# Performance work log

Hardware: AMD Instinct MI355X
Metric: run time of the kernel (lower is better)

The kernel has to match this reference:

```python
import jax, jax.numpy as jnp
import numpy as np
import math

H = 8          # num_heads
DV = 1024      # dim_V
LN_EPS = 1e-5


def _layernorm(x, g, b):
    mu = jnp.mean(x, axis=-1, keepdims=True)
    var = jnp.mean(jnp.square(x - mu), axis=-1, keepdims=True)
    return (x - mu) * jax.lax.rsqrt(var + LN_EPS) * g + b


def setup_inputs() -> dict:
    key = jax.random.key(0)
    ks = jax.random.split(key, 12)
    B, NQ, NK, DQ, DK = 4, 2048, 2048, 1024, 1024
    s = 0.02
    return {
        "Q": jax.random.normal(ks[0], (B, NQ, DQ), jnp.float32),
        "K": jax.random.normal(ks[1], (B, NK, DK), jnp.float32),
        "Wq": jax.random.normal(ks[2], (DV, DQ), jnp.float32) * s,
        "bq": jnp.zeros((DV,), jnp.float32),
        "Wk": jax.random.normal(ks[3], (DV, DK), jnp.float32) * s,
        "bk": jnp.zeros((DV,), jnp.float32),
        "Wv": jax.random.normal(ks[4], (DV, DK), jnp.float32) * s,
        "bv": jnp.zeros((DV,), jnp.float32),
        "Wo": jax.random.normal(ks[5], (DV, DV), jnp.float32) * s,
        "bo": jnp.zeros((DV,), jnp.float32),
        "g0": jnp.ones((DV,), jnp.float32),
        "b0": jnp.zeros((DV,), jnp.float32),
        "g1": jnp.ones((DV,), jnp.float32),
        "b1": jnp.zeros((DV,), jnp.float32),
    }


def reference(Q, K, Wq, bq, Wk, bk, Wv, bv, Wo, bo, g0, b0, g1, b1):
    B, NQ, _ = Q.shape
    NK = K.shape[1]
    d = DV // H  # per-head dim
    # projections
    q = (Q @ Wq.T + bq).reshape(B, NQ, H, d)
    k = (K @ Wk.T + bk).reshape(B, NK, H, d)
    v = (K @ Wv.T + bv).reshape(B, NK, H, d)
    # attention per head (split along feature dim == head split in torch code)
    logits = jnp.einsum('bqhd,bkhd->bhqk', q, k) / math.sqrt(d)
    A = jax.nn.softmax(logits, axis=-1)
    o = q + jnp.einsum('bhqk,bkhd->bqhd', A, v)  # residual with projected Q
    O = o.reshape(B, NQ, DV)
    O = _layernorm(O, g0, b0)
    O = O + jax.nn.relu(O @ Wo.T + bo)
    O = _layernorm(O, g1, b1)
    return O
```

## Files before the change

### kernel.cpp

```cpp
#include <hip/hip_runtime.h>
#include <hip/hip_bf16.h>

typedef __bf16 bf16_t;
typedef __bf16 bf16x8 __attribute__((ext_vector_type(8)));
typedef __bf16 bf16x4 __attribute__((ext_vector_type(4)));
typedef float f32x4 __attribute__((ext_vector_type(4)));

#define B_DIM 4
#define NQ 2048
#define NK 2048
#define DMODEL 1024
#define NH 8
#define DHEAD 128

#define AS1 __attribute__((address_space(1)))
#define AS3 __attribute__((address_space(3)))

__device__ __forceinline__ void gl_lds16(const void* g, void* l) {
    __builtin_amdgcn_global_load_lds((const AS1 void*)g, (AS3 void*)l, 16, 0, 0);
}

struct CvtArgs {
    const float* s[6];
    bf16_t* d[6];
    int n[6];
};

__global__ __launch_bounds__(256) void cvt_k(CvtArgs a) {
    const int p = blockIdx.y;
    const float* s = a.s[p];
    bf16_t* d = a.d[p];
    const int n = a.n[p];
    const int stride = gridDim.x * 256 * 8;
    for (int i = (blockIdx.x * 256 + threadIdx.x) * 8; i < n; i += stride) {
        float4 x0 = *(const float4*)(s + i);
        float4 x1 = *(const float4*)(s + i + 4);
        bf16x8 o = {(bf16_t)x0.x, (bf16_t)x0.y, (bf16_t)x0.z, (bf16_t)x0.w,
                    (bf16_t)x1.x, (bf16_t)x1.y, (bf16_t)x1.z, (bf16_t)x1.w};
        *(bf16x8*)(d + i) = o;
    }
}

__global__ __launch_bounds__(256) void proj_k(
    const bf16_t* Qc, const bf16_t* Kc,
    const bf16_t* Wqc, const bf16_t* Wkc, const bf16_t* Wvc,
    const float* bq, const float* bk, const float* bv,
    bf16_t* qbb, bf16_t* kbb, bf16_t* vT)
{
    const int K = DMODEL, N = DMODEL;
    const int z = blockIdx.z;
    const bf16_t* A  = (z == 0) ? Qc : Kc;
    const bf16_t* Bw = (z == 0) ? Wqc : (z == 1) ? Wkc : Wvc;
    const float* bias = (z == 0) ? bq : (z == 1) ? bk : bv;
    bf16_t* Cb = (z == 0) ? qbb : (z == 1) ? kbb : vT;

    const int tid  = threadIdx.x;
    const int lane = tid & 63;
    const int wv   = tid >> 6;
    const int l16  = lane & 15;
    const int quad = (lane >> 4) & 3;
    const int kc4  = lane >> 4;
    const int wr   = wv >> 1, wc = wv & 1;
    const int rowBase = blockIdx.y * 128;
    const int colBase = blockIdx.x * 128;

    __shared__ bf16_t sA[4096];
    __shared__ bf16_t sB[4096];

    const bf16_t* gA = A + (size_t)(rowBase + wv * 32 + l16) * K + kc4 * 8;
    const bf16_t* gB = Bw + (size_t)(colBase + wv * 32 + l16) * K + kc4 * 8;
    bf16_t* lA0 = &sA[(wv * 2) * 512];
    bf16_t* lA1 = &sA[(wv * 2 + 1) * 512];
    bf16_t* lB0 = &sB[(wv * 2) * 512];
    bf16_t* lB1 = &sB[(wv * 2 + 1) * 512];

    const f32x4 fz = {0.f, 0.f, 0.f, 0.f};
    f32x4 acc[4][4];
#pragma unroll
    for (int i = 0; i < 4; i++)
#pragma unroll
        for (int j = 0; j < 4; j++) acc[i][j] = fz;

    for (int k0 = 0; k0 < K; k0 += 32) {
        gl_lds16(gA, lA0);
        gl_lds16(gA + (size_t)16 * K, lA1);
        gl_lds16(gB, lB0);
        gl_lds16(gB + (size_t)16 * K, lB1);
        gA += 32; gB += 32;
        __syncthreads();

        bf16x8 aF[4], bF[4];
#pragma unroll
        for (int mi = 0; mi < 4; mi++)
            aF[mi] = *(const bf16x8*)(&sA[(wr * 4 + mi) * 512 + (quad * 16 + l16) * 8]);
#pragma unroll
        for (int ni = 0; ni < 4; ni++)
            bF[ni] = *(const bf16x8*)(&sB[(wc * 4 + ni) * 512 + (quad * 16 + l16) * 8]);
#pragma unroll
        for (int mi = 0; mi < 4; mi++)
#pragma unroll
            for (int ni = 0; ni < 4; ni++)
                acc[mi][ni] = __builtin_amdgcn_mfma_f32_16x16x32_bf16(
                    aF[mi], bF[ni], acc[mi][ni], 0, 0, 0);
        __syncthreads();
    }

#pragma unroll
    for (int mi = 0; mi < 4; mi++) {
#pragma unroll
        for (int ni = 0; ni < 4; ni++) {
            int row0 = rowBase + wr * 64 + mi * 16 + quad * 4;
            int col  = colBase + wc * 64 + ni * 16 + l16;
            float bvv = bias[col];
            if (z != 2) {
#pragma unroll
                for (int r = 0; r < 4; r++)
                    Cb[(size_t)(row0 + r) * N + col] = (bf16_t)(acc[mi][ni][r] + bvv);
            } else {
                int b  = row0 >> 11;
                int n0 = row0 & 2047;
                int hh = col >> 7;
                int dd = col & 127;
                bf16x4 p = {(bf16_t)(acc[mi][ni][0] + bvv), (bf16_t)(acc[mi][ni][1] + bvv),
                            (bf16_t)(acc[mi][ni][2] + bvv), (bf16_t)(acc[mi][ni][3] + bvv)};
                *(bf16x4*)(Cb + (size_t)((b * NH + hh) * DHEAD + dd) * NK + n0) = p;
            }
        }
    }
}

__global__ __launch_bounds__(256) void gemm_wo(
    const bf16_t* __restrict__ A, const bf16_t* __restrict__ Bw,
    const float* __restrict__ bias, const float* resid, float* Cf, int M, int N, int K)
{
    const int tid  = threadIdx.x;
    const int lane = tid & 63;
    const int wv   = tid >> 6;
    const int l16  = lane & 15;
    const int quad = (lane >> 4) & 3;
    const int kc4  = lane >> 4;
    const int wr   = wv >> 1, wc = wv & 1;
    const int rowBase = blockIdx.y * 128;
    const int colBase = blockIdx.x * 128;

    __shared__ bf16_t sA[4096];
    __shared__ bf16_t sB[4096];

    const bf16_t* gA = A + (size_t)(rowBase + wv * 32 + l16) * K + kc4 * 8;
    const bf16_t* gB = Bw + (size_t)(colBase + wv * 32 + l16) * K + kc4 * 8;
    bf16_t* lA0 = &sA[(wv * 2) * 512];
    bf16_t* lA1 = &sA[(wv * 2 + 1) * 512];
    bf16_t* lB0 = &sB[(wv * 2) * 512];
    bf16_t* lB1 = &sB[(wv * 2 + 1) * 512];

    const f32x4 fz = {0.f, 0.f, 0.f, 0.f};
    f32x4 acc[4][4];
#pragma unroll
    for (int i = 0; i < 4; i++)
#pragma unroll
        for (int j = 0; j < 4; j++) acc[i][j] = fz;

    for (int k0 = 0; k0 < K; k0 += 32) {
        gl_lds16(gA, lA0);
        gl_lds16(gA + (size_t)16 * K, lA1);
        gl_lds16(gB, lB0);
        gl_lds16(gB + (size_t)16 * K, lB1);
        gA += 32; gB += 32;
        __syncthreads();

        bf16x8 aF[4], bF[4];
#pragma unroll
        for (int mi = 0; mi < 4; mi++)
            aF[mi] = *(const bf16x8*)(&sA[(wr * 4 + mi) * 512 + (quad * 16 + l16) * 8]);
#pragma unroll
        for (int ni = 0; ni < 4; ni++)
            bF[ni] = *(const bf16x8*)(&sB[(wc * 4 + ni) * 512 + (quad * 16 + l16) * 8]);
#pragma unroll
        for (int mi = 0; mi < 4; mi++)
#pragma unroll
            for (int ni = 0; ni < 4; ni++)
                acc[mi][ni] = __builtin_amdgcn_mfma_f32_16x16x32_bf16(
                    aF[mi], bF[ni], acc[mi][ni], 0, 0, 0);
        __syncthreads();
    }

#pragma unroll
    for (int mi = 0; mi < 4; mi++) {
#pragma unroll
        for (int ni = 0; ni < 4; ni++) {
            int row0 = rowBase + wr * 64 + mi * 16 + quad * 4;
            int col  = colBase + wc * 64 + ni * 16 + l16;
            float bvv = bias[col];
#pragma unroll
            for (int r = 0; r < 4; r++) {
                float v = acc[mi][ni][r] + bvv;
                v = v > 0.f ? v : 0.f;
                Cf[(size_t)(row0 + r) * N + col] =
                    resid[(size_t)(row0 + r) * N + col] + v;
            }
        }
    }
}

__global__ __launch_bounds__(128, 2) void attn_k(
    const bf16_t* __restrict__ qb, const bf16_t* __restrict__ kb,
    const bf16_t* __restrict__ vT, float* __restrict__ O)
{
    const int tid  = threadIdx.x;
    const int lane = tid & 63;
    const int wv   = tid >> 6;
    const int l16  = lane & 15;
    const int quad = (lane >> 4) & 3;
    const int bh   = blockIdx.x;
    const int b    = bh >> 3;
    const int h    = bh & 7;
    const int qt   = blockIdx.y * 64;
    const int qrow0 = b * NQ + qt + wv * 32;

    __shared__ bf16_t sK[8192];
    __shared__ bf16_t sV[8192];

    bf16x8 qF[2][4];
#pragma unroll
    for (int qq = 0; qq < 2; qq++)
#pragma unroll
        for (int c = 0; c < 4; c++)
            qF[qq][c] = *(const bf16x8*)(qb + (size_t)(qrow0 + qq * 16 + l16) * DMODEL +
                                         h * DHEAD + c * 32 + quad * 8);

    const f32x4 fz = {0.f, 0.f, 0.f, 0.f};
    f32x4 accO[8][2];
#pragma unroll
    for (int db = 0; db < 8; db++)
#pragma unroll
        for (int qq = 0; qq < 2; qq++) accO[db][qq] = fz;
    float mq[2] = {-3e38f, -3e38f};
    float lq[2] = {0.f, 0.f};
    const float SC2 = 0.08838834764831845f * 1.44269504089f;

    const bf16_t* gKb = kb + ((size_t)b * NK + l16) * DMODEL + h * DHEAD + quad * 8;
    const bf16_t* gVb = vT + ((size_t)bh * DHEAD + l16) * NK + quad * 8;
    const int qa   = (quad & 1) * 2;
    const int srcA = l16 + 16 * qa;
    const int srcB = srcA + 16;
    const bool hi  = (quad >> 1) != 0;

    for (int kt = 0; kt < NK; kt += 64) {
#pragma unroll
        for (int kb2 = 0; kb2 < 2; kb2++) {
            const int kbi = wv * 2 + kb2;
#pragma unroll
            for (int c = 0; c < 4; c++)
                gl_lds16(gKb + (size_t)(kt + kbi * 16) * DMODEL + c * 32,
                         &sK[(kbi * 4 + c) * 512]);
        }
#pragma unroll
        for (int db2 = 0; db2 < 4; db2++) {
            const int dbi = wv * 4 + db2;
#pragma unroll
            for (int kc = 0; kc < 2; kc++)
                gl_lds16(gVb + (size_t)(dbi * 16) * NK + kt + kc * 32,
                         &sV[(dbi * 2 + kc) * 512]);
        }
        __syncthreads();

        f32x4 S[4][2];
#pragma unroll
        for (int kb4 = 0; kb4 < 4; kb4++) {
            S[kb4][0] = fz; S[kb4][1] = fz;
#pragma unroll
            for (int c = 0; c < 4; c++) {
                bf16x8 kF = *(const bf16x8*)(&sK[(kb4 * 4 + c) * 512 + lane * 8]);
                S[kb4][0] = __builtin_amdgcn_mfma_f32_16x16x32_bf16(kF, qF[0][c], S[kb4][0], 0, 0, 0);
                S[kb4][1] = __builtin_amdgcn_mfma_f32_16x16x32_bf16(kF, qF[1][c], S[kb4][1], 0, 0, 0);
            }
        }

        float alph[2];
#pragma unroll
        for (int qq = 0; qq < 2; qq++) {
            float mx = fmaxf(fmaxf(fmaxf(S[0][qq][0], S[0][qq][1]), fmaxf(S[0][qq][2], S[0][qq][3])),
                       fmaxf(fmaxf(S[1][qq][0], S[1][qq][1]), fmaxf(S[1][qq][2], S[1][qq][3])));
            mx = fmaxf(mx, fmaxf(fmaxf(fmaxf(S[2][qq][0], S[2][qq][1]), fmaxf(S[2][qq][2], S[2][qq][3])),
                           fmaxf(fmaxf(S[3][qq][0], S[3][qq][1]), fmaxf(S[3][qq][2], S[3][qq][3]))));
            mx = fmaxf(mx, __shfl_xor(mx, 16));
            mx = fmaxf(mx, __shfl_xor(mx, 32));
            float mn = fmaxf(mq[qq], mx);
            float al = exp2f((mq[qq] - mn) * SC2);
            mq[qq] = mn;
            float mc = mn * SC2;
            float sum = 0.f;
#pragma unroll
            for (int kb4 = 0; kb4 < 4; kb4++)
#pragma unroll
                for (int r = 0; r < 4; r++) {
                    float p = exp2f(fmaf(S[kb4][qq][r], SC2, -mc));
                    S[kb4][qq][r] = p;
                    sum += p;
                }
            lq[qq] = lq[qq] * al + sum;
            alph[qq] = al;
        }
#pragma unroll
        for (int db = 0; db < 8; db++)
#pragma unroll
            for (int qq = 0; qq < 2; qq++)
#pragma unroll
                for (int r = 0; r < 4; r++) accO[db][qq][r] *= alph[qq];

        uint2 pk[4][2];
#pragma unroll
        for (int kb4 = 0; kb4 < 4; kb4++)
#pragma unroll
            for (int qq = 0; qq < 2; qq++) {
                bf16x4 t = {(bf16_t)S[kb4][qq][0], (bf16_t)S[kb4][qq][1],
                            (bf16_t)S[kb4][qq][2], (bf16_t)S[kb4][qq][3]};
                pk[kb4][qq] = __builtin_bit_cast(uint2, t);
            }
        bf16x8 pF[2][2];
#pragma unroll
        for (int kc = 0; kc < 2; kc++)
#pragma unroll
            for (int qq = 0; qq < 2; qq++) {
                unsigned a0 = (unsigned)__shfl((int)pk[2 * kc][qq].x, srcA);
                unsigned b0 = (unsigned)__shfl((int)pk[2 * kc + 1][qq].x, srcA);
                unsigned a1 = (unsigned)__shfl((int)pk[2 * kc][qq].y, srcA);
                unsigned b1 = (unsigned)__shfl((int)pk[2 * kc + 1][qq].y, srcA);
                unsigned a2 = (unsigned)__shfl((int)pk[2 * kc][qq].x, srcB);
                unsigned b2 = (unsigned)__shfl((int)pk[2 * kc + 1][qq].x, srcB);
                unsigned a3 = (unsigned)__shfl((int)pk[2 * kc][qq].y, srcB);
                unsigned b3 = (unsigned)__shfl((int)pk[2 * kc + 1][qq].y, srcB);
                uint4 w = {hi ? b0 : a0, hi ? b1 : a1, hi ? b2 : a2, hi ? b3 : a3};
                pF[kc][qq] = __builtin_bit_cast(bf16x8, w);
            }

#pragma unroll
        for (int kc = 0; kc < 2; kc++)
#pragma unroll
            for (int db = 0; db < 8; db++) {
                bf16x8 vF = *(const bf16x8*)(&sV[(db * 2 + kc) * 512 + lane * 8]);
                accO[db][0] = __builtin_amdgcn_mfma_f32_16x16x32_bf16(vF, pF[kc][0], accO[db][0], 0, 0, 0);
                accO[db][1] = __builtin_amdgcn_mfma_f32_16x16x32_bf16(vF, pF[kc][1], accO[db][1], 0, 0, 0);
            }
        __syncthreads();
    }

    float inv[2];
#pragma unroll
    for (int qq = 0; qq < 2; qq++) {
        float s = lq[qq];
        s += __shfl_xor(s, 16);
        s += __shfl_xor(s, 32);
        inv[qq] = 1.0f / s;
    }

#pragma unroll
    for (int qq = 0; qq < 2; qq++) {
        const int grow = qrow0 + qq * 16 + l16;
#pragma unroll
        for (int db = 0; db < 8; db++) {
            const int gcol = h * DHEAD + db * 16 + quad * 4;
            bf16x4 qr = *(const bf16x4*)(qb + (size_t)grow * DMODEL + gcol);
            f32x4 o;
#pragma unroll
            for (int r = 0; r < 4; r++)
                o[r] = accO[db][qq][r] * inv[qq] + (float)qr[r];
            *(f32x4*)(O + (size_t)grow * DMODEL + gcol) = o;
        }
    }
}

__global__ __launch_bounds__(256) void ln_k(
    const float* __restrict__ X, const float* __restrict__ g,
    const float* __restrict__ bta, float* __restrict__ Yf, bf16_t* Yb)
{
    const int row = blockIdx.x;
    const int t = threadIdx.x;
    float4 x = *(const float4*)(X + (size_t)row * DMODEL + t * 4);
    float s  = x.x + x.y + x.z + x.w;
    float sq = x.x * x.x + x.y * x.y + x.z * x.z + x.w * x.w;
#pragma unroll
    for (int o = 1; o < 64; o <<= 1) {
        s  += __shfl_xor(s, o);
        sq += __shfl_xor(sq, o);
    }
    __shared__ float ls[8];
    int w = t >> 6, ln = t & 63;
    if (ln == 0) { ls[w] = s; ls[4 + w] = sq; }
    __syncthreads();
    s  = ls[0] + ls[1] + ls[2] + ls[3];
    sq = ls[4] + ls[5] + ls[6] + ls[7];
    float mu  = s * (1.f / DMODEL);
    float var = sq * (1.f / DMODEL) - mu * mu;
    float rs  = rsqrtf(var + 1e-5f);
    float4 gv = *(const float4*)(g + t * 4);
    float4 bv = *(const float4*)(bta + t * 4);
    float4 y;
    y.x = (x.x - mu) * rs * gv.x + bv.x;
    y.y = (x.y - mu) * rs * gv.y + bv.y;
    y.z = (x.z - mu) * rs * gv.z + bv.z;
    y.w = (x.w - mu) * rs * gv.w + bv.w;
    *(float4*)(Yf + (size_t)row * DMODEL + t * 4) = y;
    if (Yb) {
        bf16x4 yb = {(bf16_t)y.x, (bf16_t)y.y, (bf16_t)y.z, (bf16_t)y.w};
        *(bf16x4*)(Yb + (size_t)row * DMODEL + t * 4) = yb;
    }
}

extern "C" void kernel_launch(void* const* d_in, const int* in_sizes, int n_in,
                              void* d_out, int out_size, void* d_ws, size_t ws_size,
                              hipStream_t stream)
{
    const float* Q  = (const float*)d_in[0];
    const float* Kx = (const float*)d_in[1];
    const float* Wq = (const float*)d_in[2];
    const float* bq = (const float*)d_in[3];
    const float* Wk = (const float*)d_in[4];
    const float* bk = (const float*)d_in[5];
    const float* Wv = (const float*)d_in[6];
    const float* bv = (const float*)d_in[7];
    const float* Wo = (const float*)d_in[8];
    const float* bo = (const float*)d_in[9];
    const float* g0 = (const float*)d_in[10];
    const float* b0 = (const float*)d_in[11];
    const float* g1 = (const float*)d_in[12];
    const float* b1 = (const float*)d_in[13];
    float* out = (float*)d_out;

    char* ws = (char*)d_ws;
    bf16_t* Qc  = (bf16_t*)(ws);
    bf16_t* Kc  = (bf16_t*)(ws + 16777216);
    bf16_t* Wqc = (bf16_t*)(ws + 33554432);
    bf16_t* Wkc = (bf16_t*)(ws + 35651584);
    bf16_t* Wvc = (bf16_t*)(ws + 37748736);
    bf16_t* Woc = (bf16_t*)(ws + 39845888);
    bf16_t* qbb = (bf16_t*)(ws + 41943040);
    bf16_t* kbb = (bf16_t*)(ws + 58720256);
    bf16_t* vT  = (bf16_t*)(ws + 75497472);
    float*  Obuf = (float*)(ws + 92274688);
    float*  Lf  = (float*)(ws);
    bf16_t* Lb  = kbb;

    CvtArgs ca;
    ca.s[0] = Q;  ca.d[0] = Qc;  ca.n[0] = B_DIM * NQ * DMODEL;
    ca.s[1] = Kx; ca.d[1] = Kc;  ca.n[1] = B_DIM * NK * DMODEL;
    ca.s[2] = Wq; ca.d[2] = Wqc; ca.n[2] = DMODEL * DMODEL;
    ca.s[3] = Wk; ca.d[3] = Wkc; ca.n[3] = DMODEL * DMODEL;
    ca.s[4] = Wv; ca.d[4] = Wvc; ca.n[4] = DMODEL * DMODEL;
    ca.s[5] = Wo; ca.d[5] = Woc; ca.n[5] = DMODEL * DMODEL;
    cvt_k<<<dim3(512, 6), 256, 0, stream>>>(ca);

    const int M = B_DIM * NQ;

    proj_k<<<dim3(DMODEL / 128, M / 128, 3), 256, 0, stream>>>(
        Qc, Kc, Wqc, Wkc, Wvc, bq, bk, bv, qbb, kbb, vT);

    attn_k<<<dim3(B_DIM * NH, NQ / 64), 128, 0, stream>>>(qbb, kbb, vT, Obuf);

    ln_k<<<dim3(M), 256, 0, stream>>>(Obuf, g0, b0, Lf, Lb);

    gemm_wo<<<dim3(DMODEL / 128, M / 128), 256, 0, stream>>>(
        Lb, Woc, bo, Lf, Lf, M, DMODEL, DMODEL);

    ln_k<<<dim3(M), 256, 0, stream>>>(Lf, g1, b1, out, nullptr);
}
```

Baseline: 460.8 us.

## Double-buffer B/K tiles in LDS and load A/V operands directly from global

The GEMM kernels are merged into a templated core. Only the weight tile is staged through LDS, now double-buffered with the next tile's async load issued before the current compute, and A fragments are read straight from global into registers. The attention kernel likewise double-buffers K tiles in LDS and loads V fragments directly from global, cutting one barrier per iteration. The aim is to overlap memory latency with MFMA work and halve synchronization, at the cost of uncoalesced global register loads and more register pressure.

Result: slower. 564.1 us (+22.4%).

```diff
diff --git a/kernel.cpp b/kernel.cpp
--- a/kernel.cpp
+++ b/kernel.cpp
@@ -41,19 +41,12 @@
     }
 }
 
-__global__ __launch_bounds__(256) void proj_k(
-    const bf16_t* Qc, const bf16_t* Kc,
-    const bf16_t* Wqc, const bf16_t* Wkc, const bf16_t* Wvc,
-    const float* bq, const float* bk, const float* bv,
-    bf16_t* qbb, bf16_t* kbb, bf16_t* vT)
-{
-    const int K = DMODEL, N = DMODEL;
-    const int z = blockIdx.z;
-    const bf16_t* A  = (z == 0) ? Qc : Kc;
-    const bf16_t* Bw = (z == 0) ? Wqc : (z == 1) ? Wkc : Wvc;
-    const float* bias = (z == 0) ? bq : (z == 1) ? bk : bv;
-    bf16_t* Cb = (z == 0) ? qbb : (z == 1) ? kbb : vT;
-
+template <int MODE>
+__device__ __forceinline__ void gemm_core(
+    const bf16_t* A, const bf16_t* Bw, const float* bias, const float* resid,
+    bf16_t* Cb, float* Cf, int N, int rowBase, int colBase, bf16_t (*sB)[4096])
+{
+    const int K = DMODEL;
     const int tid  = threadIdx.x;
     const int lane = tid & 63;
     const int wv   = tid >> 6;
@@ -61,18 +54,9 @@
     const int quad = (lane >> 4) & 3;
     const int kc4  = lane >> 4;
     const int wr   = wv >> 1, wc = wv & 1;
-    const int rowBase = blockIdx.y * 128;
-    const int colBase = blockIdx.x * 128;
-
-    __shared__ bf16_t sA[4096];
-    __shared__ bf16_t sB[4096];
-
-    const bf16_t* gA = A + (size_t)(rowBase + wv * 32 + l16) * K + kc4 * 8;
+
     const bf16_t* gB = Bw + (size_t)(colBase + wv * 32 + l16) * K + kc4 * 8;
-    bf16_t* lA0 = &sA[(wv * 2) * 512];
-    bf16_t* lA1 = &sA[(wv * 2 + 1) * 512];
-    bf16_t* lB0 = &sB[(wv * 2) * 512];
-    bf16_t* lB1 = &sB[(wv * 2 + 1) * 512];
+    const bf16_t* gA = A + (size_t)(rowBase + wr * 64 + l16) * K + quad * 8;
 
     const f32x4 fz = {0.f, 0.f, 0.f, 0.f};
     f32x4 acc[4][4];
@@ -81,28 +65,32 @@
 #pragma unroll
         for (int j = 0; j < 4; j++) acc[i][j] = fz;
 
-    for (int k0 = 0; k0 < K; k0 += 32) {
-        gl_lds16(gA, lA0);
-        gl_lds16(gA + (size_t)16 * K, lA1);
-        gl_lds16(gB, lB0);
-        gl_lds16(gB + (size_t)16 * K, lB1);
-        gA += 32; gB += 32;
+    gl_lds16(gB,                  &sB[0][(wv * 2) * 512]);
+    gl_lds16(gB + (size_t)16 * K, &sB[0][(wv * 2 + 1) * 512]);
+    gB += 32;
+
+    for (int t = 0; t < 32; t++) {
         __syncthreads();
-
-        bf16x8 aF[4], bF[4];
+        const int cur = t & 1;
+        bf16x8 aF[4];
 #pragma unroll
         for (int mi = 0; mi < 4; mi++)
-            aF[mi] = *(const bf16x8*)(&sA[(wr * 4 + mi) * 512 + (quad * 16 + l16) * 8]);
+            aF[mi] = *(const bf16x8*)(gA + (size_t)mi * 16 * K + t * 32);
+        if (t + 1 < 32) {
+            gl_lds16(gB,                  &sB[cur ^ 1][(wv * 2) * 512]);
+            gl_lds16(gB + (size_t)16 * K, &sB[cur ^ 1][(wv * 2 + 1) * 512]);
+            gB += 32;
+        }
+        bf16x8 bF[4];
 #pragma unroll
         for (int ni = 0; ni < 4; ni++)
-            bF[ni] = *(const bf16x8*)(&sB[(wc * 4 + ni) * 512 + (quad * 16 + l16) * 8]);
+            bF[ni] = *(const bf16x8*)(&sB[cur][(wc * 4 + ni) * 512 + (quad * 16 + l16) * 8]);
 #pragma unroll
         for (int mi = 0; mi < 4; mi++)
 #pragma unroll
             for (int ni = 0; ni < 4; ni++)
                 acc[mi][ni] = __builtin_amdgcn_mfma_f32_16x16x32_bf16(
                     aF[mi], bF[ni], acc[mi][ni], 0, 0, 0);
-        __syncthreads();
     }
 
 #pragma unroll
@@ -112,10 +100,18 @@
             int row0 = rowBase + wr * 64 + mi * 16 + quad * 4;
             int col  = colBase + wc * 64 + ni * 16 + l16;
             float bvv = bias[col];
-            if (z != 2) {
+            if (MODE == 0) {
 #pragma unroll
                 for (int r = 0; r < 4; r++)
                     Cb[(size_t)(row0 + r) * N + col] = (bf16_t)(acc[mi][ni][r] + bvv);
+            } else if (MODE == 1) {
+#pragma unroll
+                for (int r = 0; r < 4; r++) {
+                    float v = acc[mi][ni][r] + bvv;
+                    v = v > 0.f ? v : 0.f;
+                    Cf[(size_t)(row0 + r) * N + col] =
+                        resid[(size_t)(row0 + r) * N + col] + v;
+                }
             } else {
                 int b  = row0 >> 11;
                 int n0 = row0 & 2047;
@@ -129,77 +125,31 @@
     }
 }
 
+__global__ __launch_bounds__(256) void proj_k(
+    const bf16_t* Qc, const bf16_t* Kc,
+    const bf16_t* Wqc, const bf16_t* Wkc, const bf16_t* Wvc,
+    const float* bq, const float* bk, const float* bv,
+    bf16_t* qbb, bf16_t* kbb, bf16_t* vT)
+{
+    __shared__ bf16_t sB[2][4096];
+    const int z = blockIdx.z;
+    const int rowBase = blockIdx.y * 128;
+    const int colBase = blockIdx.x * 128;
+    if (z == 0)
+        gemm_core<0>(Qc, Wqc, bq, nullptr, qbb, nullptr, DMODEL, rowBase, colBase, sB);
+    else if (z == 1)
+        gemm_core<0>(Kc, Wkc, bk, nullptr, kbb, nullptr, DMODEL, rowBase, colBase, sB);
+    else
+        gemm_core<2>(Kc, Wvc, bv, nullptr, vT, nullptr, DMODEL, rowBase, colBase, sB);
+}
+
 __global__ __launch_bounds__(256) void gemm_wo(
     const bf16_t* __restrict__ A, const bf16_t* __restrict__ Bw,
-    const float* __restrict__ bias, const float* resid, float* Cf, int M, int N, int K)
-{
-    const int tid  = threadIdx.x;
-    const int lane = tid & 63;
-    const int wv   = tid >> 6;
-    const int l16  = lane & 15;
-    const int quad = (lane >> 4) & 3;
-    const int kc4  = lane >> 4;
-    const int wr   = wv >> 1, wc = wv & 1;
-    const int rowBase = blockIdx.y * 128;
-    const int colBase = blockIdx.x * 128;
-
-    __shared__ bf16_t sA[4096];
-    __shared__ bf16_t sB[4096];
-
-    const bf16_t* gA = A + (size_t)(rowBase + wv * 32 + l16) * K + kc4 * 8;
-    const bf16_t* gB = Bw + (size_t)(colBase + wv * 32 + l16) * K + kc4 * 8;
-    bf16_t* lA0 = &sA[(wv * 2) * 512];
-    bf16_t* lA1 = &sA[(wv * 2 + 1) * 512];
-    bf16_t* lB0 = &sB[(wv * 2) * 512];
-    bf16_t* lB1 = &sB[(wv * 2 + 1) * 512];
-
-    const f32x4 fz = {0.f, 0.f, 0.f, 0.f};
-    f32x4 acc[4][4];
-#pragma unroll
-    for (int i = 0; i < 4; i++)
-#pragma unroll
-        for (int j = 0; j < 4; j++) acc[i][j] = fz;
-
-    for (int k0 = 0; k0 < K; k0 += 32) {
-        gl_lds16(gA, lA0);
-        gl_lds16(gA + (size_t)16 * K, lA1);
-        gl_lds16(gB, lB0);
-        gl_lds16(gB + (size_t)16 * K, lB1);
-        gA += 32; gB += 32;
-        __syncthreads();
-
-        bf16x8 aF[4], bF[4];
-#pragma unroll
-        for (int mi = 0; mi < 4; mi++)
-            aF[mi] = *(const bf16x8*)(&sA[(wr * 4 + mi) * 512 + (quad * 16 + l16) * 8]);
-#pragma unroll
-        for (int ni = 0; ni < 4; ni++)
-            bF[ni] = *(const bf16x8*)(&sB[(wc * 4 + ni) * 512 + (quad * 16 + l16) * 8]);
-#pragma unroll
-        for (int mi = 0; mi < 4; mi++)
-#pragma unroll
-            for (int ni = 0; ni < 4; ni++)
-                acc[mi][ni] = __builtin_amdgcn_mfma_f32_16x16x32_bf16(
-                    aF[mi], bF[ni], acc[mi][ni], 0, 0, 0);
-        __syncthreads();
-    }
-
-#pragma unroll
-    for (int mi = 0; mi < 4; mi++) {
-#pragma unroll
-        for (int ni = 0; ni < 4; ni++) {
-            int row0 = rowBase + wr * 64 + mi * 16 + quad * 4;
-            int col  = colBase + wc * 64 + ni * 16 + l16;
-            float bvv = bias[col];
-#pragma unroll
-            for (int r = 0; r < 4; r++) {
-                float v = acc[mi][ni][r] + bvv;
-                v = v > 0.f ? v : 0.f;
-                Cf[(size_t)(row0 + r) * N + col] =
-                    resid[(size_t)(row0 + r) * N + col] + v;
-            }
-        }
-    }
+    const float* __restrict__ bias, const float* resid, float* Cf)
+{
+    __shared__ bf16_t sB[2][4096];
+    gemm_core<1>(A, Bw, bias, resid, nullptr, Cf, DMODEL,
+                 blockIdx.y * 128, blockIdx.x * 128, sB);
 }
 
 __global__ __launch_bounds__(128, 2) void attn_k(
@@ -217,8 +167,7 @@
     const int qt   = blockIdx.y * 64;
     const int qrow0 = b * NQ + qt + wv * 32;
 
-    __shared__ bf16_t sK[8192];
-    __shared__ bf16_t sV[8192];
+    __shared__ bf16_t sK[2][8192];
 
     bf16x8 qF[2][4];
 #pragma unroll
@@ -245,24 +194,37 @@
     const int srcB = srcA + 16;
     const bool hi  = (quad >> 1) != 0;
 
-    for (int kt = 0; kt < NK; kt += 64) {
-#pragma unroll
-        for (int kb2 = 0; kb2 < 2; kb2++) {
-            const int kbi = wv * 2 + kb2;
-#pragma unroll
-            for (int c = 0; c < 4; c++)
-                gl_lds16(gKb + (size_t)(kt + kbi * 16) * DMODEL + c * 32,
-                         &sK[(kbi * 4 + c) * 512]);
-        }
-#pragma unroll
-        for (int db2 = 0; db2 < 4; db2++) {
-            const int dbi = wv * 4 + db2;
+#pragma unroll
+    for (int kb2 = 0; kb2 < 2; kb2++) {
+        const int kbi = wv * 2 + kb2;
+#pragma unroll
+        for (int c = 0; c < 4; c++)
+            gl_lds16(gKb + (size_t)(kbi * 16) * DMODEL + c * 32, &sK[0][(kbi * 4 + c) * 512]);
+    }
+
+    for (int it = 0; it < NK / 64; it++) {
+        __syncthreads();
+        const int cur = it & 1;
+        const int kt = it * 64;
+
+        bf16x8 vF[8][2];
+#pragma unroll
+        for (int db = 0; db < 8; db++)
 #pragma unroll
             for (int kc = 0; kc < 2; kc++)
-                gl_lds16(gVb + (size_t)(dbi * 16) * NK + kt + kc * 32,
-                         &sV[(dbi * 2 + kc) * 512]);
-        }
-        __syncthreads();
+                vF[db][kc] = *(const bf16x8*)(gVb + (size_t)(db * 16) * NK + kt + kc * 32);
+
+        if (it + 1 < NK / 64) {
+            const size_t ko = (size_t)(kt + 64);
+#pragma unroll
+            for (int kb2 = 0; kb2 < 2; kb2++) {
+                const int kbi = wv * 2 + kb2;
+#pragma unroll
+                for (int c = 0; c < 4; c++)
+                    gl_lds16(gKb + (ko + kbi * 16) * DMODEL + c * 32,
+                             &sK[cur ^ 1][(kbi * 4 + c) * 512]);
+            }
+        }
 
         f32x4 S[4][2];
 #pragma unroll
@@ -270,7 +232,7 @@
             S[kb4][0] = fz; S[kb4][1] = fz;
 #pragma unroll
             for (int c = 0; c < 4; c++) {
-                bf16x8 kF = *(const bf16x8*)(&sK[(kb4 * 4 + c) * 512 + lane * 8]);
+                bf16x8 kF = *(const bf16x8*)(&sK[cur][(kb4 * 4 + c) * 512 + lane * 8]);
                 S[kb4][0] = __builtin_amdgcn_mfma_f32_16x16x32_bf16(kF, qF[0][c], S[kb4][0], 0, 0, 0);
                 S[kb4][1] = __builtin_amdgcn_mfma_f32_16x16x32_bf16(kF, qF[1][c], S[kb4][1], 0, 0, 0);
             }
@@ -338,11 +300,9 @@
         for (int kc = 0; kc < 2; kc++)
 #pragma unroll
             for (int db = 0; db < 8; db++) {
-                bf16x8 vF = *(const bf16x8*)(&sV[(db * 2 + kc) * 512 + lane * 8]);
-                accO[db][0] = __builtin_amdgcn_mfma_f32_16x16x32_bf16(vF, pF[kc][0], accO[db][0], 0, 0, 0);
-                accO[db][1] = __builtin_amdgcn_mfma_f32_16x16x32_bf16(vF, pF[kc][1], accO[db][1], 0, 0, 0);
-            }
-        __syncthreads();
+                accO[db][0] = __builtin_amdgcn_mfma_f32_16x16x32_bf16(vF[db][kc], pF[kc][0], accO[db][0], 0, 0, 0);
+                accO[db][1] = __builtin_amdgcn_mfma_f32_16x16x32_bf16(vF[db][kc], pF[kc][1], accO[db][1], 0, 0, 0);
+            }
     }
 
     float inv[2];
@@ -459,8 +419,7 @@
 
     ln_k<<<dim3(M), 256, 0, stream>>>(Obuf, g0, b0, Lf, Lb);
 
-    gemm_wo<<<dim3(DMODEL / 128, M / 128), 256, 0, stream>>>(
-        Lb, Woc, bo, Lf, Lf, M, DMODEL, DMODEL);
+    gemm_wo<<<dim3(DMODEL / 128, M / 128), 256, 0, stream>>>(Lb, Woc, bo, Lf, Lf);
 
     ln_k<<<dim3(M), 256, 0, stream>>>(Lf, g1, b1, out, nullptr);
 }
```
